# Optimization experiments

Measured on AMD Instinct MI355X. Metric: run time of the kernel, lower is better.

Reference implementation:

```python
import jax, jax.numpy as jnp
import numpy as np

ALPHA = -1.0  # config['dist_to_logits_alpha']
N_EMB = 1024
D = 256
BSZ, TSZ = 16, 2048


def setup_inputs() -> dict:
    key = jax.random.key(0)
    k1, k2 = jax.random.split(key)
    x = jax.random.normal(k1, (BSZ, TSZ, D), dtype=jnp.float32)
    # nn.init.uniform_(embedding, a=-1.0, b=1.0), shape (1, n_embeddings, embedding_dim)
    embedding = jax.random.uniform(k2, (1, N_EMB, D), dtype=jnp.float32, minval=-1.0, maxval=1.0)
    return {"x": x, "embedding": embedding}


def reference(x, embedding):
    bsz, tsz, csz = x.shape
    emb = embedding[0]                      # [M, D]
    M = emb.shape[0]
    x_flat = x.reshape(-1, csz)             # [N, D], N = bsz*tsz

    distances = (jnp.sum(emb ** 2, axis=1)[None, :]
                 + jnp.sum(x_flat ** 2, axis=1, keepdims=True)
                 - 2.0 * (x_flat @ emb.T))          # [N, M]
    logits = ALPHA * distances                       # [N, M] (groups == 1)

    k = jnp.argmax(logits, axis=-1)                  # [N]
    hard_x = jax.nn.one_hot(k, M, dtype=logits.dtype)  # [N, M]

    hard_probs = jnp.mean(hard_x, axis=0)            # [M]
    code_perplexity = -jnp.sum(hard_probs * jnp.log2(hard_probs + 1e-10))

    avg_probs = jnp.mean(jax.nn.softmax(logits, axis=-1), axis=0)  # [M]
    prob_perplexity = -jnp.sum(avg_probs * jnp.log2(avg_probs + 1e-10))

    # eval path: distances_map = hard_x -> quantized = one_hot @ emb == gather
    quantized = jnp.take(emb, k, axis=0).reshape(bsz, tsz, -1)  # [B, T, D]
    quantization_inds = k.reshape(bsz, tsz, 1)                  # groups == 1

    commitment_loss = jnp.mean((x - quantized) ** 2)

    return quantized, code_perplexity, prob_perplexity, quantization_inds, commitment_loss
```

## Files before the change

kernel.cpp:

```cpp
#include <hip/hip_runtime.h>
#include <stdint.h>

#define N_ROWS   32768
#define M_CODES  1024
#define D_DIM    256
#define BN       64
#define NBLOCKS  (N_ROWS / BN)
#define EPS      1.0f
#define CAND_MAX 16

#define OFF_Q      0
#define OFF_CODEP  8388608
#define OFF_PROBP  8388609
#define OFF_INDS   8388610
#define OFF_COMMIT 8421378

typedef __attribute__((ext_vector_type(8))) short bf16x8;
typedef __attribute__((ext_vector_type(8))) unsigned short u16x8;
typedef __attribute__((ext_vector_type(4))) float f32x4;

__device__ __forceinline__ unsigned short f2bf(float f) {
    unsigned int u = __float_as_uint(f);
    u += 0x7FFFu + ((u >> 16) & 1u);
    return (unsigned short)(u >> 16);
}

__global__ __launch_bounds__(64) void vq_prep(
    const float* __restrict__ emb,
    unsigned short* __restrict__ efrag, float* __restrict__ enorm,
    float* __restrict__ pprobs_g, unsigned int* __restrict__ counts_g,
    float* __restrict__ commit_g)
{
    const int r = blockIdx.x, t = threadIdx.x;

    if (t < 32) {
        const float4 a = *(const float4*)(emb + r * D_DIM + t * 8);
        const float4 b = *(const float4*)(emb + r * D_DIM + t * 8 + 4);
        u16x8 H;
        H[0] = f2bf(a.x); H[1] = f2bf(a.y); H[2] = f2bf(a.z); H[3] = f2bf(a.w);
        H[4] = f2bf(b.x); H[5] = f2bf(b.y); H[6] = f2bf(b.z); H[7] = f2bf(b.w);
        const int off = (((r >> 4) * 8 + (t >> 2)) * 64 + (((t & 3) << 4) | (r & 15))) * 8;
        *(u16x8*)(efrag + off) = H;
    }

    const float4 v = *(const float4*)(emb + r * D_DIM + t * 4);
    float n = v.x * v.x + v.y * v.y + v.z * v.z + v.w * v.w;
    #pragma unroll
    for (int off = 32; off; off >>= 1) n += __shfl_xor(n, off);
    if (t == 0) {
        enorm[r] = n;
        pprobs_g[r] = 0.0f;
        counts_g[r] = 0u;
        if (r == 0) commit_g[0] = 0.0f;
    }
}

__global__ __launch_bounds__(1024, 4) void vq_main(
    const float* __restrict__ xg, const float* __restrict__ embf,
    const unsigned short* __restrict__ efrag, const float* __restrict__ enorm,
    float* __restrict__ pprobs_g, unsigned int* __restrict__ counts_g,
    float* __restrict__ commit_g,
    float* __restrict__ out_q, float* __restrict__ out_inds)
{
    __shared__ char  xs[32768];
    __shared__ float wmin[16][64];
    __shared__ float wsum[16][64];
    __shared__ float rmin[64];
    __shared__ float rinv[64];
    __shared__ int   cand[64][CAND_MAX];
    __shared__ int   ccnt[64];
    __shared__ int   kidx[64];

    const int tid  = threadIdx.x;
    const int wave = tid >> 6, lane = tid & 63;
    const int lrow = lane & 15, lg = lane >> 4;
    const int sw   = (lrow & 7) << 4;
    const int row0 = blockIdx.x * BN;
    const int wc0  = wave * 64;

    {
        const int row = tid >> 4, kc = tid & 15;
        const float* xr = xg + (size_t)(row0 + row) * D_DIM + kc * 16;
        const float4 v0 = *(const float4*)(xr);
        const float4 v1 = *(const float4*)(xr + 4);
        const float4 v2 = *(const float4*)(xr + 8);
        const float4 v3 = *(const float4*)(xr + 12);
        u16x8 H0, H1;
        H0[0] = f2bf(v0.x); H0[1] = f2bf(v0.y); H0[2] = f2bf(v0.z); H0[3] = f2bf(v0.w);
        H0[4] = f2bf(v1.x); H0[5] = f2bf(v1.y); H0[6] = f2bf(v1.z); H0[7] = f2bf(v1.w);
        H1[0] = f2bf(v2.x); H1[1] = f2bf(v2.y); H1[2] = f2bf(v2.z); H1[3] = f2bf(v2.w);
        H1[4] = f2bf(v3.x); H1[5] = f2bf(v3.y); H1[6] = f2bf(v3.z); H1[7] = f2bf(v3.w);
        const int rsw = (row & 7) << 4;
        *(u16x8*)(xs + ((row * 512 + kc * 32) ^ rsw))      = H0;
        *(u16x8*)(xs + ((row * 512 + kc * 32 + 16) ^ rsw)) = H1;
        if (tid < 64) ccnt[tid] = 0;
    }
    __syncthreads();

    f32x4 acc[4][4];
    #pragma unroll
    for (int rf = 0; rf < 4; ++rf)
        #pragma unroll
        for (int cf = 0; cf < 4; ++cf)
            acc[rf][cf] = (f32x4){0.f, 0.f, 0.f, 0.f};

    const char* bbase = (const char*)efrag + lane * 16 + wave * 32768;
    #pragma unroll
    for (int ks = 0; ks < 8; ++ks) {
        bf16x8 a[4];
        #pragma unroll
        for (int rf = 0; rf < 4; ++rf)
            a[rf] = *(const bf16x8*)(xs + (((rf * 16 + lrow) * 512 + ks * 64 + lg * 16) ^ sw));
        #pragma unroll
        for (int cf = 0; cf < 4; ++cf) {
            const bf16x8 b = *(const bf16x8*)(bbase + cf * 8192 + ks * 1024);
            acc[0][cf] = __builtin_amdgcn_mfma_f32_16x16x32_bf16(a[0], b, acc[0][cf], 0, 0, 0);
            acc[1][cf] = __builtin_amdgcn_mfma_f32_16x16x32_bf16(a[1], b, acc[1][cf], 0, 0, 0);
            acc[2][cf] = __builtin_amdgcn_mfma_f32_16x16x32_bf16(a[2], b, acc[2][cf], 0, 0, 0);
            acc[3][cf] = __builtin_amdgcn_mfma_f32_16x16x32_bf16(a[3], b, acc[3][cf], 0, 0, 0);
        }
    }

    #pragma unroll
    for (int cf = 0; cf < 4; ++cf) {
        const float en = enorm[wc0 + cf * 16 + lrow];
        #pragma unroll
        for (int rf = 0; rf < 4; ++rf)
            #pragma unroll
            for (int j = 0; j < 4; ++j)
                acc[rf][cf][j] = en - 2.0f * acc[rf][cf][j];
    }

    #pragma unroll
    for (int rf = 0; rf < 4; ++rf) {
        #pragma unroll
        for (int j = 0; j < 4; ++j) {
            const int row = rf * 16 + lg * 4 + j;
            float m = fminf(fminf(acc[rf][0][j], acc[rf][1][j]),
                            fminf(acc[rf][2][j], acc[rf][3][j]));
            m = fminf(m, __shfl_xor(m, 1));
            m = fminf(m, __shfl_xor(m, 2));
            m = fminf(m, __shfl_xor(m, 4));
            m = fminf(m, __shfl_xor(m, 8));
            if (lrow == 0) wmin[wave][row] = m;
        }
    }
    __syncthreads();

    {
        const int row = wave * 4 + lg;
        float m = wmin[lrow][row];
        m = fminf(m, __shfl_xor(m, 1));
        m = fminf(m, __shfl_xor(m, 2));
        m = fminf(m, __shfl_xor(m, 4));
        m = fminf(m, __shfl_xor(m, 8));
        if (lrow == 0) rmin[row] = m;
    }
    __syncthreads();

    #pragma unroll
    for (int rf = 0; rf < 4; ++rf) {
        #pragma unroll
        for (int j = 0; j < 4; ++j) {
            const int row = rf * 16 + lg * 4 + j;
            const float m = rmin[row];
            float s = 0.f;
            #pragma unroll
            for (int cf = 0; cf < 4; ++cf) {
                const float d = acc[rf][cf][j];
                if (d <= m + EPS) {
                    const int pos = atomicAdd(&ccnt[row], 1);
                    if (pos < CAND_MAX) cand[row][pos] = wc0 + cf * 16 + lrow;
                }
                s += __expf(m - d);
            }
            s += __shfl_xor(s, 1); s += __shfl_xor(s, 2);
            s += __shfl_xor(s, 4); s += __shfl_xor(s, 8);
            if (lrow == 0) wsum[wave][row] = s;
        }
    }
    __syncthreads();

    {
        const int row = wave * 4 + lg;
        float s = wsum[lrow][row];
        s += __shfl_xor(s, 1); s += __shfl_xor(s, 2);
        s += __shfl_xor(s, 4); s += __shfl_xor(s, 8);
        if (lrow == 0) rinv[row] = 1.0f / s;

        for (int q = 0; q < 4; ++q) {
            const int r  = wave * 4 + q;
            const int rg = row0 + r;
            const int n  = min(ccnt[r], CAND_MAX);
            const float4 x4 = *(const float4*)(xg + (size_t)rg * D_DIM + lane * 4);
            float best = 3.4e38f; int bcol = 0x7fffffff;
            for (int i = 0; i < n; ++i) {
                const int c = cand[r][i];
                const float4 e4 = *(const float4*)(embf + (size_t)c * D_DIM + lane * 4);
                float dt = x4.x * e4.x + x4.y * e4.y + x4.z * e4.z + x4.w * e4.w;
                dt += __shfl_xor(dt, 1);  dt += __shfl_xor(dt, 2);
                dt += __shfl_xor(dt, 4);  dt += __shfl_xor(dt, 8);
                dt += __shfl_xor(dt, 16); dt += __shfl_xor(dt, 32);
                const float t = enorm[c] - 2.0f * dt;
                if (t < best || (t == best && c < bcol)) { best = t; bcol = c; }
            }
            if (lane == 0) {
                kidx[r] = bcol;
                out_inds[rg] = (float)bcol;
                atomicAdd(&counts_g[bcol], 1u);
            }
        }
    }
    __syncthreads();

    #pragma unroll
    for (int cf = 0; cf < 4; ++cf) {
        float t = 0.f;
        #pragma unroll
        for (int rf = 0; rf < 4; ++rf)
            #pragma unroll
            for (int j = 0; j < 4; ++j) {
                const int row = rf * 16 + lg * 4 + j;
                t += __expf(rmin[row] - acc[rf][cf][j]) * rinv[row];
            }
        t += __shfl_xor(t, 16);
        t += __shfl_xor(t, 32);
        if (lg == 0) unsafeAtomicAdd(&pprobs_g[wc0 + cf * 16 + lrow], t);
    }

    {
        float cacc = 0.f;
        for (int q = 0; q < 4; ++q) {
            const int r  = wave * 4 + q;
            const int rg = row0 + r;
            const int ki = kidx[r];
            const float4 e4 = *(const float4*)(embf + (size_t)ki * D_DIM + lane * 4);
            const float4 x4 = *(const float4*)(xg + (size_t)rg * D_DIM + lane * 4);
            *(float4*)(out_q + (size_t)rg * D_DIM + lane * 4) = e4;
            const float dx = x4.x - e4.x, dy = x4.y - e4.y;
            const float dz = x4.z - e4.z, dw = x4.w - e4.w;
            cacc += dx * dx + dy * dy + dz * dz + dw * dw;
        }
        cacc += __shfl_xor(cacc, 1);  cacc += __shfl_xor(cacc, 2);
        cacc += __shfl_xor(cacc, 4);  cacc += __shfl_xor(cacc, 8);
        cacc += __shfl_xor(cacc, 16); cacc += __shfl_xor(cacc, 32);
        if (lane == 0) unsafeAtomicAdd(commit_g, cacc);
    }
}

__global__ __launch_bounds__(1024) void vq_final(
    const float* __restrict__ pprobs_g, const unsigned int* __restrict__ counts_g,
    const float* __restrict__ commit_g, float* __restrict__ out)
{
    __shared__ float red1[16], red2[16];
    const int tid = threadIdx.x, wave = tid >> 6, lane = tid & 63;

    const float p_hard = (float)counts_g[tid] * (1.0f / (float)N_ROWS);
    float t1 = p_hard * log2f(p_hard + 1e-10f);
    const float p_avg = pprobs_g[tid] * (1.0f / (float)N_ROWS);
    float t2 = p_avg * log2f(p_avg + 1e-10f);

    #pragma unroll
    for (int off = 32; off; off >>= 1) { t1 += __shfl_xor(t1, off); t2 += __shfl_xor(t2, off); }
    if (lane == 0) { red1[wave] = t1; red2[wave] = t2; }
    __syncthreads();
    if (tid == 0) {
        float s1 = 0.0f, s2 = 0.0f;
        #pragma unroll
        for (int i = 0; i < 16; ++i) { s1 += red1[i]; s2 += red2[i]; }
        out[OFF_CODEP]  = -s1;
        out[OFF_PROBP]  = -s2;
        out[OFF_COMMIT] = commit_g[0] * (1.0f / (float)(N_ROWS * D_DIM));
    }
}

extern "C" void kernel_launch(void* const* d_in, const int* in_sizes, int n_in,
                              void* d_out, int out_size, void* d_ws, size_t ws_size,
                              hipStream_t stream)
{
    (void)in_sizes; (void)n_in; (void)out_size; (void)ws_size;
    const float* xg   = (const float*)d_in[0];
    const float* embf = (const float*)d_in[1];
    float* out = (float*)d_out;

    char* ws = (char*)d_ws;
    unsigned short* efrag    = (unsigned short*)(ws);
    float*          enorm    = (float*)(ws + 524288);
    float*          pprobs_g = (float*)(ws + 528384);
    unsigned int*   counts_g = (unsigned int*)(ws + 532480);
    float*          commit_g = (float*)(ws + 536576);

    hipLaunchKernelGGL(vq_prep, dim3(M_CODES), dim3(64), 0, stream,
                       embf, efrag, enorm, pprobs_g, counts_g, commit_g);

    hipLaunchKernelGGL(vq_main, dim3(NBLOCKS), dim3(1024), 0, stream,
                       xg, embf, efrag, enorm, pprobs_g, counts_g, commit_g,
                       out + OFF_Q, out + OFF_INDS);

    hipLaunchKernelGGL(vq_final, dim3(1), dim3(1024), 0, stream,
                       pprobs_g, counts_g, commit_g, out);
}
```

Before: 220.5 us.

## Restructure VQ main kernel: 32-row blocks, register-resident A, double-buffered B fragments

Halves the rows per block to 32 and uses 8 waves of 512 threads, each covering 128 codes. The x tile is now converted to bf16 directly into registers instead of being staged through LDS, and the codebook fragments are double-buffered in registers so their loads overlap the MFMA work. The quantized-row write and the commitment loss are folded into the candidate-rescoring loop, which drops the separate gather pass and the kidx buffer. In exchange, register pressure rises, codebook fragments are reloaded twice as often across the grid, and occupancy changes with the new launch bounds.

```diff
diff --git a/kernel.cpp b/kernel.cpp
--- a/kernel.cpp
+++ b/kernel.cpp
@@ -1,10 +1,11 @@
 #include <hip/hip_runtime.h>
+#include <hip/hip_bf16.h>
 #include <stdint.h>
 
 #define N_ROWS   32768
 #define M_CODES  1024
 #define D_DIM    256
-#define BN       64
+#define BN       32
 #define NBLOCKS  (N_ROWS / BN)
 #define EPS      1.0f
 #define CAND_MAX 16
@@ -20,9 +21,8 @@
 typedef __attribute__((ext_vector_type(4))) float f32x4;
 
 __device__ __forceinline__ unsigned short f2bf(float f) {
-    unsigned int u = __float_as_uint(f);
-    u += 0x7FFFu + ((u >> 16) & 1u);
-    return (unsigned short)(u >> 16);
+    __hip_bfloat16 h = __float2bfloat16(f);
+    return __builtin_bit_cast(unsigned short, h);
 }
 
 __global__ __launch_bounds__(64) void vq_prep(
@@ -55,89 +55,97 @@
     }
 }
 
-__global__ __launch_bounds__(1024, 4) void vq_main(
+__global__ __launch_bounds__(512, 2) void vq_main(
     const float* __restrict__ xg, const float* __restrict__ embf,
     const unsigned short* __restrict__ efrag, const float* __restrict__ enorm,
     float* __restrict__ pprobs_g, unsigned int* __restrict__ counts_g,
     float* __restrict__ commit_g,
     float* __restrict__ out_q, float* __restrict__ out_inds)
 {
-    __shared__ char  xs[32768];
-    __shared__ float wmin[16][64];
-    __shared__ float wsum[16][64];
-    __shared__ float rmin[64];
-    __shared__ float rinv[64];
-    __shared__ int   cand[64][CAND_MAX];
-    __shared__ int   ccnt[64];
-    __shared__ int   kidx[64];
+    __shared__ float wmin[8][32];
+    __shared__ float wsum[8][32];
+    __shared__ float rmin[32];
+    __shared__ float rinv[32];
+    __shared__ int   cand[32][CAND_MAX];
+    __shared__ int   ccnt[32];
 
     const int tid  = threadIdx.x;
     const int wave = tid >> 6, lane = tid & 63;
     const int lrow = lane & 15, lg = lane >> 4;
-    const int sw   = (lrow & 7) << 4;
     const int row0 = blockIdx.x * BN;
-    const int wc0  = wave * 64;
-
-    {
-        const int row = tid >> 4, kc = tid & 15;
-        const float* xr = xg + (size_t)(row0 + row) * D_DIM + kc * 16;
-        const float4 v0 = *(const float4*)(xr);
-        const float4 v1 = *(const float4*)(xr + 4);
-        const float4 v2 = *(const float4*)(xr + 8);
-        const float4 v3 = *(const float4*)(xr + 12);
-        u16x8 H0, H1;
-        H0[0] = f2bf(v0.x); H0[1] = f2bf(v0.y); H0[2] = f2bf(v0.z); H0[3] = f2bf(v0.w);
-        H0[4] = f2bf(v1.x); H0[5] = f2bf(v1.y); H0[6] = f2bf(v1.z); H0[7] = f2bf(v1.w);
-        H1[0] = f2bf(v2.x); H1[1] = f2bf(v2.y); H1[2] = f2bf(v2.z); H1[3] = f2bf(v2.w);
-        H1[4] = f2bf(v3.x); H1[5] = f2bf(v3.y); H1[6] = f2bf(v3.z); H1[7] = f2bf(v3.w);
-        const int rsw = (row & 7) << 4;
-        *(u16x8*)(xs + ((row * 512 + kc * 32) ^ rsw))      = H0;
-        *(u16x8*)(xs + ((row * 512 + kc * 32 + 16) ^ rsw)) = H1;
-        if (tid < 64) ccnt[tid] = 0;
-    }
-    __syncthreads();
-
-    f32x4 acc[4][4];
-    #pragma unroll
-    for (int rf = 0; rf < 4; ++rf)
-        #pragma unroll
-        for (int cf = 0; cf < 4; ++cf)
+    const int wc0  = wave * 128;
+
+    if (tid < 32) ccnt[tid] = 0;
+
+    const char* bb = (const char*)efrag + wave * 65536 + lane * 16;
+    bf16x8 bA[8], bB[8];
+    #pragma unroll
+    for (int ks = 0; ks < 8; ++ks)
+        bA[ks] = *(const bf16x8*)(bb + ks * 1024);
+
+    bf16x8 a[2][8];
+    #pragma unroll
+    for (int rf = 0; rf < 2; ++rf) {
+        const float* xr = xg + (size_t)(row0 + rf * 16 + lrow) * D_DIM + lg * 8;
+        #pragma unroll
+        for (int ks = 0; ks < 8; ++ks) {
+            const float4 v0 = *(const float4*)(xr + ks * 32);
+            const float4 v1 = *(const float4*)(xr + ks * 32 + 4);
+            u16x8 H;
+            H[0] = f2bf(v0.x); H[1] = f2bf(v0.y); H[2] = f2bf(v0.z); H[3] = f2bf(v0.w);
+            H[4] = f2bf(v1.x); H[5] = f2bf(v1.y); H[6] = f2bf(v1.z); H[7] = f2bf(v1.w);
+            a[rf][ks] = __builtin_bit_cast(bf16x8, H);
+        }
+    }
+
+    f32x4 acc[2][8];
+    #pragma unroll
+    for (int rf = 0; rf < 2; ++rf)
+        #pragma unroll
+        for (int cf = 0; cf < 8; ++cf)
             acc[rf][cf] = (f32x4){0.f, 0.f, 0.f, 0.f};
 
-    const char* bbase = (const char*)efrag + lane * 16 + wave * 32768;
-    #pragma unroll
-    for (int ks = 0; ks < 8; ++ks) {
-        bf16x8 a[4];
-        #pragma unroll
-        for (int rf = 0; rf < 4; ++rf)
-            a[rf] = *(const bf16x8*)(xs + (((rf * 16 + lrow) * 512 + ks * 64 + lg * 16) ^ sw));
-        #pragma unroll
-        for (int cf = 0; cf < 4; ++cf) {
-            const bf16x8 b = *(const bf16x8*)(bbase + cf * 8192 + ks * 1024);
-            acc[0][cf] = __builtin_amdgcn_mfma_f32_16x16x32_bf16(a[0], b, acc[0][cf], 0, 0, 0);
-            acc[1][cf] = __builtin_amdgcn_mfma_f32_16x16x32_bf16(a[1], b, acc[1][cf], 0, 0, 0);
-            acc[2][cf] = __builtin_amdgcn_mfma_f32_16x16x32_bf16(a[2], b, acc[2][cf], 0, 0, 0);
-            acc[3][cf] = __builtin_amdgcn_mfma_f32_16x16x32_bf16(a[3], b, acc[3][cf], 0, 0, 0);
-        }
-    }
-
-    #pragma unroll
-    for (int cf = 0; cf < 4; ++cf) {
+    #pragma unroll
+    for (int cfp = 0; cfp < 4; ++cfp) {
+        const int cfe = 2 * cfp, cfo = 2 * cfp + 1;
+        #pragma unroll
+        for (int ks = 0; ks < 8; ++ks)
+            bB[ks] = *(const bf16x8*)(bb + cfo * 8192 + ks * 1024);
+        #pragma unroll
+        for (int ks = 0; ks < 8; ++ks) {
+            acc[0][cfe] = __builtin_amdgcn_mfma_f32_16x16x32_bf16(a[0][ks], bA[ks], acc[0][cfe], 0, 0, 0);
+            acc[1][cfe] = __builtin_amdgcn_mfma_f32_16x16x32_bf16(a[1][ks], bA[ks], acc[1][cfe], 0, 0, 0);
+        }
+        if (cfp < 3) {
+            #pragma unroll
+            for (int ks = 0; ks < 8; ++ks)
+                bA[ks] = *(const bf16x8*)(bb + (cfe + 2) * 8192 + ks * 1024);
+        }
+        #pragma unroll
+        for (int ks = 0; ks < 8; ++ks) {
+            acc[0][cfo] = __builtin_amdgcn_mfma_f32_16x16x32_bf16(a[0][ks], bB[ks], acc[0][cfo], 0, 0, 0);
+            acc[1][cfo] = __builtin_amdgcn_mfma_f32_16x16x32_bf16(a[1][ks], bB[ks], acc[1][cfo], 0, 0, 0);
+        }
+    }
+
+    #pragma unroll
+    for (int cf = 0; cf < 8; ++cf) {
         const float en = enorm[wc0 + cf * 16 + lrow];
         #pragma unroll
-        for (int rf = 0; rf < 4; ++rf)
+        for (int rf = 0; rf < 2; ++rf)
             #pragma unroll
             for (int j = 0; j < 4; ++j)
                 acc[rf][cf][j] = en - 2.0f * acc[rf][cf][j];
     }
 
     #pragma unroll
-    for (int rf = 0; rf < 4; ++rf) {
+    for (int rf = 0; rf < 2; ++rf) {
         #pragma unroll
         for (int j = 0; j < 4; ++j) {
             const int row = rf * 16 + lg * 4 + j;
-            float m = fminf(fminf(acc[rf][0][j], acc[rf][1][j]),
-                            fminf(acc[rf][2][j], acc[rf][3][j]));
+            float m = acc[rf][0][j];
+            #pragma unroll
+            for (int cf = 1; cf < 8; ++cf) m = fminf(m, acc[rf][cf][j]);
             m = fminf(m, __shfl_xor(m, 1));
             m = fminf(m, __shfl_xor(m, 2));
             m = fminf(m, __shfl_xor(m, 4));
@@ -149,24 +157,23 @@
 
     {
         const int row = wave * 4 + lg;
-        float m = wmin[lrow][row];
+        float m = wmin[lrow & 7][row];
         m = fminf(m, __shfl_xor(m, 1));
         m = fminf(m, __shfl_xor(m, 2));
         m = fminf(m, __shfl_xor(m, 4));
-        m = fminf(m, __shfl_xor(m, 8));
         if (lrow == 0) rmin[row] = m;
     }
     __syncthreads();
 
     #pragma unroll
-    for (int rf = 0; rf < 4; ++rf) {
+    for (int rf = 0; rf < 2; ++rf) {
         #pragma unroll
         for (int j = 0; j < 4; ++j) {
             const int row = rf * 16 + lg * 4 + j;
             const float m = rmin[row];
             float s = 0.f;
             #pragma unroll
-            for (int cf = 0; cf < 4; ++cf) {
+            for (int cf = 0; cf < 8; ++cf) {
                 const float d = acc[rf][cf][j];
                 if (d <= m + EPS) {
                     const int pos = atomicAdd(&ccnt[row], 1);
@@ -181,11 +188,11 @@
     }
     __syncthreads();
 
+    float cacc = 0.f;
     {
         const int row = wave * 4 + lg;
-        float s = wsum[lrow][row];
-        s += __shfl_xor(s, 1); s += __shfl_xor(s, 2);
-        s += __shfl_xor(s, 4); s += __shfl_xor(s, 8);
+        float s = wsum[lrow & 7][row];
+        s += __shfl_xor(s, 1); s += __shfl_xor(s, 2); s += __shfl_xor(s, 4);
         if (lrow == 0) rinv[row] = 1.0f / s;
 
         for (int q = 0; q < 4; ++q) {
@@ -194,6 +201,7 @@
             const int n  = min(ccnt[r], CAND_MAX);
             const float4 x4 = *(const float4*)(xg + (size_t)rg * D_DIM + lane * 4);
             float best = 3.4e38f; int bcol = 0x7fffffff;
+            float4 be4 = (float4){0.f, 0.f, 0.f, 0.f};
             for (int i = 0; i < n; ++i) {
                 const int c = cand[r][i];
                 const float4 e4 = *(const float4*)(embf + (size_t)c * D_DIM + lane * 4);
@@ -202,10 +210,13 @@
                 dt += __shfl_xor(dt, 4);  dt += __shfl_xor(dt, 8);
                 dt += __shfl_xor(dt, 16); dt += __shfl_xor(dt, 32);
                 const float t = enorm[c] - 2.0f * dt;
-                if (t < best || (t == best && c < bcol)) { best = t; bcol = c; }
+                if (t < best || (t == best && c < bcol)) { best = t; bcol = c; be4 = e4; }
             }
+            *(float4*)(out_q + (size_t)rg * D_DIM + lane * 4) = be4;
+            const float dx = x4.x - be4.x, dy = x4.y - be4.y;
+            const float dz = x4.z - be4.z, dw = x4.w - be4.w;
+            cacc += dx * dx + dy * dy + dz * dz + dw * dw;
             if (lane == 0) {
-                kidx[r] = bcol;
                 out_inds[rg] = (float)bcol;
                 atomicAdd(&counts_g[bcol], 1u);
             }
@@ -213,39 +224,32 @@
     }
     __syncthreads();
 
-    #pragma unroll
-    for (int cf = 0; cf < 4; ++cf) {
+    float rm[2][4], ri[2][4];
+    #pragma unroll
+    for (int rf = 0; rf < 2; ++rf)
+        #pragma unroll
+        for (int j = 0; j < 4; ++j) {
+            const int row = rf * 16 + lg * 4 + j;
+            rm[rf][j] = rmin[row];
+            ri[rf][j] = rinv[row];
+        }
+    #pragma unroll
+    for (int cf = 0; cf < 8; ++cf) {
         float t = 0.f;
         #pragma unroll
-        for (int rf = 0; rf < 4; ++rf)
-            #pragma unroll
-            for (int j = 0; j < 4; ++j) {
-                const int row = rf * 16 + lg * 4 + j;
-                t += __expf(rmin[row] - acc[rf][cf][j]) * rinv[row];
-            }
+        for (int rf = 0; rf < 2; ++rf)
+            #pragma unroll
+            for (int j = 0; j < 4; ++j)
+                t += __expf(rm[rf][j] - acc[rf][cf][j]) * ri[rf][j];
         t += __shfl_xor(t, 16);
         t += __shfl_xor(t, 32);
         if (lg == 0) unsafeAtomicAdd(&pprobs_g[wc0 + cf * 16 + lrow], t);
     }
 
-    {
-        float cacc = 0.f;
-        for (int q = 0; q < 4; ++q) {
-            const int r  = wave * 4 + q;
-            const int rg = row0 + r;
-            const int ki = kidx[r];
-            const float4 e4 = *(const float4*)(embf + (size_t)ki * D_DIM + lane * 4);
-            const float4 x4 = *(const float4*)(xg + (size_t)rg * D_DIM + lane * 4);
-            *(float4*)(out_q + (size_t)rg * D_DIM + lane * 4) = e4;
-            const float dx = x4.x - e4.x, dy = x4.y - e4.y;
-            const float dz = x4.z - e4.z, dw = x4.w - e4.w;
-            cacc += dx * dx + dy * dy + dz * dz + dw * dw;
-        }
-        cacc += __shfl_xor(cacc, 1);  cacc += __shfl_xor(cacc, 2);
-        cacc += __shfl_xor(cacc, 4);  cacc += __shfl_xor(cacc, 8);
-        cacc += __shfl_xor(cacc, 16); cacc += __shfl_xor(cacc, 32);
-        if (lane == 0) unsafeAtomicAdd(commit_g, cacc);
-    }
+    cacc += __shfl_xor(cacc, 1);  cacc += __shfl_xor(cacc, 2);
+    cacc += __shfl_xor(cacc, 4);  cacc += __shfl_xor(cacc, 8);
+    cacc += __shfl_xor(cacc, 16); cacc += __shfl_xor(cacc, 32);
+    if (lane == 0) unsafeAtomicAdd(commit_g, cacc);
 }
 
 __global__ __launch_bounds__(1024) void vq_final(
@@ -293,7 +297,7 @@
     hipLaunchKernelGGL(vq_prep, dim3(M_CODES), dim3(64), 0, stream,
                        embf, efrag, enorm, pprobs_g, counts_g, commit_g);
 
-    hipLaunchKernelGGL(vq_main, dim3(NBLOCKS), dim3(1024), 0, stream,
+    hipLaunchKernelGGL(vq_main, dim3(NBLOCKS), dim3(512), 0, stream,
                        xg, embf, efrag, enorm, pprobs_g, counts_g, commit_g,
                        out + OFF_Q, out + OFF_INDS);
 
```

Result: no change. 221.1 us (+0.3%).
